# Optimization experiments

Measured on AMD Instinct MI355X. Metric: run time of the kernel, lower is better.

## Reference

```python
import jax, jax.numpy as jnp
import numpy as np

F_, H_, W_ = 6, 16, 28          # latent video grid (frames, height, width)
DIM, NH = 1536, 12
HD = DIM // NH                   # 128
L = F_ * H_ * W_                 # 2688 tokens
EPS = 1e-6
BLOCK = 3 * H_ * W_              # block_causal_size = 3*frame_height*frame_width


def setup_inputs() -> dict:
    key = jax.random.key(0)
    ks = jax.random.split(key, 8)
    def lin(k):
        return jax.random.normal(k, (DIM, DIM), jnp.float32) * 0.02
    x = jax.random.normal(ks[0], (1, L, DIM), jnp.float32)
    # RoPE freqs: unit-modulus complex numbers stored as [...,(re,im)]
    ang = jax.random.uniform(ks[1], (1024, HD // 2), jnp.float32, -np.pi, np.pi)
    freqs = jnp.stack([jnp.cos(ang), jnp.sin(ang)], axis=-1)  # [1024, 64, 2]
    return {
        'x': x,
        'seq_lens': jnp.array([L], jnp.int32),
        'grid_sizes': jnp.array([[F_, H_, W_]], jnp.int32),
        'freqs': freqs,
        'Wq': lin(ks[2]), 'bq': jnp.zeros((DIM,), jnp.float32),
        'Wk': lin(ks[3]), 'bk': jnp.zeros((DIM,), jnp.float32),
        'Wv': lin(ks[4]), 'bv': jnp.zeros((DIM,), jnp.float32),
        'Wo': lin(ks[5]), 'bo': jnp.zeros((DIM,), jnp.float32),
        'gq': jnp.ones((DIM,), jnp.float32),
        'gk': jnp.ones((DIM,), jnp.float32),
    }


def _rmsnorm(x, g):
    # WanRMSNorm: x * rsqrt(mean(x^2) + eps) * weight
    return x * jax.lax.rsqrt(jnp.mean(x * x, axis=-1, keepdims=True) + EPS) * g


def _rope_apply(x, F, H, W, freqs, start_frame=0):
    # x: [B, L, n, d]; freqs: [1024, d//2, 2] (re, im). Per-axis split [c0, c3, c3].
    B, Lx, n, d = x.shape
    c = d // 2
    c3 = c // 3
    c0 = c - 2 * c3
    f0 = freqs[start_frame:start_frame + F, :c0]      # [F, c0, 2]
    f1 = freqs[:H, c0:c0 + c3]                        # [H, c3, 2]
    f2 = freqs[:W, c0 + c3:]                          # [W, c3, 2]
    ff = jnp.concatenate([
        jnp.broadcast_to(f0[:, None, None], (F, H, W, c0, 2)),
        jnp.broadcast_to(f1[None, :, None], (F, H, W, c3, 2)),
        jnp.broadcast_to(f2[None, None, :], (F, H, W, c3, 2)),
    ], axis=3).reshape(Lx, 1, c, 2)                   # [L, 1, c, 2]
    xr = x.reshape(B, Lx, n, c, 2)
    xre, xim = xr[..., 0], xr[..., 1]
    fre, fim = ff[None, ..., 0], ff[None, ..., 1]     # broadcast over batch, heads
    ore = xre * fre - xim * fim
    oim = xre * fim + xim * fre
    return jnp.stack([ore, oim], axis=-1).reshape(B, Lx, n, d)


def reference(x, seq_lens, grid_sizes, freqs, Wq, bq, Wk, bk, Wv, bv, Wo, bo, gq, gk):
    b, s = x.shape[:2]
    F = int(grid_sizes[0, 0]); H = int(grid_sizes[0, 1]); W = int(grid_sizes[0, 2])
    q = _rmsnorm(x @ Wq + bq, gq).reshape(b, s, NH, HD)
    k = _rmsnorm(x @ Wk + bk, gk).reshape(b, s, NH, HD)
    v = (x @ Wv + bv).reshape(b, s, NH, HD)
    rq = _rope_apply(q, F, H, W, freqs)
    rk = _rope_apply(k, F, H, W, freqs)
    # block-causal attention: query attends to keys in same-or-earlier 3-frame block
    scores = jnp.einsum('bihd,bjhd->bhij', rq, rk) * (HD ** -0.5)
    blk = jnp.arange(s) // (3 * H * W)
    mask = blk[None, :] <= blk[:, None]               # [s, s]
    scores = jnp.where(mask[None, None], scores, -1e30)
    attn = jax.nn.softmax(scores, axis=-1)
    out = jnp.einsum('bhij,bjhd->bihd', attn, v).reshape(b, s, DIM)
    return out @ Wo + bo
```

## Files before the change

kernel.cpp:

```cpp
#include <hip/hip_runtime.h>

#define L_SEQ 2688
#define DIM   1536
#define NH    12
#define HD    128
#define BLK_TOK 1344
#define HW_   448
#define W_    28

typedef unsigned short u16;
typedef unsigned int   u32;
typedef __attribute__((ext_vector_type(4))) float f32x4;
typedef __attribute__((ext_vector_type(16))) float f32x16;
typedef __attribute__((ext_vector_type(8))) short s16x8;
typedef __attribute__((ext_vector_type(2))) int i32x2;
typedef __attribute__((ext_vector_type(4))) u32 u32x4;

__device__ __forceinline__ u16 f2b(float f) {
    u32 u = __builtin_bit_cast(u32, f);
    return (u16)((u + 0x7FFFu + ((u >> 16) & 1u)) >> 16);
}
__device__ __forceinline__ float b2f(u16 b) {
    return __builtin_bit_cast(float, (u32)b << 16);
}
__device__ __forceinline__ u32 cvt_pk_bf16(float lo, float hi) {
    u32 r;
    asm("v_cvt_pk_bf16_f32 %0, %1, %2" : "=v"(r) : "v"(lo), "v"(hi));
    return r;
}

__global__ __launch_bounds__(256) void k_cvt_x(const float* __restrict__ x,
                                               u16* __restrict__ xb, int n4) {
    int i = blockIdx.x * 256 + threadIdx.x;
    int stride = gridDim.x * 256;
    for (; i < n4; i += stride) {
        float4 v = ((const float4*)x)[i];
        ushort4 o;
        o.x = f2b(v.x); o.y = f2b(v.y); o.z = f2b(v.z); o.w = f2b(v.w);
        ((ushort4*)xb)[i] = o;
    }
}

__global__ __launch_bounds__(256) void k_trans_w(const float* __restrict__ w0,
                                                 const float* __restrict__ w1,
                                                 const float* __restrict__ w2,
                                                 const float* __restrict__ w3,
                                                 u16* __restrict__ wt_all) {
    const float* w = blockIdx.z == 0 ? w0 : blockIdx.z == 1 ? w1 : blockIdx.z == 2 ? w2 : w3;
    u16* wt = wt_all + (size_t)blockIdx.z * DIM * DIM;
    __shared__ float t[64][65];
    const int k0 = blockIdx.y * 64, n0 = blockIdx.x * 64;
    const int c = threadIdx.x & 63, rg = threadIdx.x >> 6;
#pragma unroll
    for (int it = 0; it < 16; ++it) {
        int r = rg * 16 + it;
        t[r][c] = w[(size_t)(k0 + r) * DIM + n0 + c];
    }
    __syncthreads();
#pragma unroll
    for (int it = 0; it < 16; ++it) {
        int r = rg * 16 + it;
        wt[(size_t)(n0 + r) * DIM + k0 + c] = f2b(t[c][r]);
    }
}

template<int OUTF>
__global__ __launch_bounds__(256, 2) void k_gemm(const u16* __restrict__ A,
                                                 const u16* __restrict__ Bt_all,
                                                 const float* __restrict__ b0,
                                                 const float* __restrict__ b1,
                                                 const float* __restrict__ b2,
                                                 void* __restrict__ out_all) {
    const int z = blockIdx.z;
    const u16* Bt = Bt_all + (size_t)z * DIM * DIM;
    const float* bias = z == 0 ? b0 : z == 1 ? b1 : b2;

    __shared__ u16 lA[128 * 32];
    __shared__ u16 lB[128 * 32];
    const int tid = threadIdx.x, lane = tid & 63, wid = tid >> 6;
    const int wm = wid >> 1, wn = wid & 1;
    const int bm = blockIdx.y, bn = blockIdx.x;
    const int lr = lane & 15, lg = lane >> 4;

    f32x4 acc[4][4] = {};

    for (int kt = 0; kt < DIM / 32; ++kt) {
#pragma unroll
        for (int i = 0; i < 2; ++i) {
            int s = wid * 128 + i * 64 + lane;
            int row = s >> 2, c16 = s & 3;
            const u16* ga = A + (size_t)(bm * 128 + row) * DIM + kt * 32 + c16 * 8;
            __builtin_amdgcn_global_load_lds(
                (const __attribute__((address_space(1))) u32*)ga,
                (__attribute__((address_space(3))) u32*)&lA[(wid * 128 + i * 64) * 8],
                16, 0, 0);
            const u16* gb = Bt + (size_t)(bn * 128 + row) * DIM + kt * 32 + c16 * 8;
            __builtin_amdgcn_global_load_lds(
                (const __attribute__((address_space(1))) u32*)gb,
                (__attribute__((address_space(3))) u32*)&lB[(wid * 128 + i * 64) * 8],
                16, 0, 0);
        }
        __syncthreads();
        s16x8 af[4], bf[4];
#pragma unroll
        for (int m = 0; m < 4; ++m)
            af[m] = *(const s16x8*)&lA[(wm * 64 + m * 16 + lr) * 32 + lg * 8];
#pragma unroll
        for (int n = 0; n < 4; ++n)
            bf[n] = *(const s16x8*)&lB[(wn * 64 + n * 16 + lr) * 32 + lg * 8];
#pragma unroll
        for (int m = 0; m < 4; ++m)
#pragma unroll
            for (int n = 0; n < 4; ++n)
                acc[m][n] = __builtin_amdgcn_mfma_f32_16x16x32_bf16(af[m], bf[n], acc[m][n], 0, 0, 0);
        __syncthreads();
    }
#pragma unroll
    for (int n = 0; n < 4; ++n) {
        int col = bn * 128 + wn * 64 + n * 16 + lr;
        float bv = bias[col];
#pragma unroll
        for (int m = 0; m < 4; ++m) {
            int row0 = bm * 128 + wm * 64 + m * 16 + lg * 4;
#pragma unroll
            for (int r = 0; r < 4; ++r) {
                float v = acc[m][n][r] + bv;
                if (OUTF)
                    ((float*)out_all)[(size_t)(row0 + r) * DIM + col] = v;
                else
                    ((u16*)out_all)[(size_t)z * L_SEQ * DIM + (size_t)(row0 + r) * DIM + col] = f2b(v);
            }
        }
    }
}

__global__ __launch_bounds__(256) void k_norm_rope(const u16* __restrict__ pre_all,
                                                   const float* __restrict__ gq,
                                                   const float* __restrict__ gk,
                                                   const float* __restrict__ freqs,
                                                   u16* __restrict__ qh,
                                                   u16* __restrict__ kh) {
    const int which = blockIdx.y;
    const u16* pre = pre_all + (size_t)which * L_SEQ * DIM;
    const float* g = which ? gk : gq;
    u16* outh = which ? kh : qh;

    const int i = blockIdx.x;
    const int t = threadIdx.x;
    const u32* prow = (const u32*)(pre + (size_t)i * DIM);

    float re[3], im[3];
    float ss = 0.f;
#pragma unroll
    for (int a = 0; a < 3; ++a) {
        u32 p = prow[t + a * 256];
        float x = b2f((u16)(p & 0xFFFFu)), y = b2f((u16)(p >> 16));
        re[a] = x; im[a] = y;
        ss += x * x + y * y;
    }
#pragma unroll
    for (int o = 32; o > 0; o >>= 1) ss += __shfl_down(ss, o, 64);
    __shared__ float sred[4];
    if ((t & 63) == 0) sred[t >> 6] = ss;
    __syncthreads();
    float rms = rsqrtf((sred[0] + sred[1] + sred[2] + sred[3]) * (1.0f / DIM) + 1e-6f);

    const int f = i / HW_;
    const int rem = i - f * HW_;
    const int hp = rem / W_;
    const int wp = rem - hp * W_;
#pragma unroll
    for (int a = 0; a < 3; ++a) {
        int j = t + a * 256;
        int h = j >> 6, pj = j & 63;
        float2 gg = ((const float2*)g)[j];
        float x = re[a] * rms * gg.x;
        float y = im[a] * rms * gg.y;
        int ridx = pj < 22 ? f : (pj < 43 ? hp : wp);
        float2 cs = ((const float2*)freqs)[ridx * 64 + pj];
        float ore = x * cs.x - y * cs.y;
        float oim = x * cs.y + y * cs.x;
        u32 o = (u32)f2b(ore) | ((u32)f2b(oim) << 16);
        ((u32*)outh)[(size_t)h * (L_SEQ * 64) + (size_t)i * 64 + pj] = o;
    }
}

__global__ __launch_bounds__(256) void k_vtrans(const u16* __restrict__ vpre,
                                                u16* __restrict__ vt) {
    const int i0 = blockIdx.x * 64, d0 = blockIdx.y * 64, h = blockIdx.z;
    __shared__ u16 t[64][68];
    const int c = threadIdx.x & 63, rg = threadIdx.x >> 6;
#pragma unroll
    for (int it = 0; it < 16; ++it) {
        int r = rg * 16 + it;
        t[r][c] = vpre[(size_t)(i0 + r) * DIM + h * HD + d0 + c];
    }
    __syncthreads();
#pragma unroll
    for (int it = 0; it < 16; ++it) {
        int r = rg * 16 + it;
        vt[(size_t)h * (HD * L_SEQ) + (size_t)(d0 + r) * L_SEQ + i0 + c] = t[c][r];
    }
}

__global__ __launch_bounds__(256, 2) void k_attn(const u16* __restrict__ qh,
                                                 const u16* __restrict__ kh,
                                                 const u16* __restrict__ vt,
                                                 u16* __restrict__ ob,
                                                 float* __restrict__ Opart,
                                                 float* __restrict__ mlp) {
    __shared__ char lsm[2][32768];

    const int flat = blockIdx.x;
    const int xcd = flat & 7, idx = flat >> 3;
    const int work = (xcd < 4) ? (xcd * 95 + idx) : (380 + (xcd - 4) * 94 + idx);
    const int head = work / 63;
    const int bx = work - head * 63;
    int qt, kv0, mode;
    if (bx < 21)      { qt = bx;      kv0 = 0;  mode = 0; }
    else if (bx < 42) { qt = bx;      kv0 = 0;  mode = 1; }
    else              { qt = bx - 21; kv0 = 21; mode = 2; }

    const int tid = threadIdx.x, lane = tid & 63, w = tid >> 6;
    const int pairI = w >> 1;
    const int qhalf = w & 1;
    const int q31 = lane & 31, hi = lane >> 5;
    const size_t hOff = (size_t)head * ((size_t)L_SEQ * HD);
    const u16* Kh = kh + hOff;
    const u16* Vh = vt + hOff;
    const int qrow0 = qt * 64 + qhalf * 32;

    s16x8 aq[8];
#pragma unroll
    for (int kk = 0; kk < 8; ++kk)
        aq[kk] = *(const s16x8*)&qh[hOff + (size_t)(qrow0 + q31) * HD + kk * 16 + hi * 8];

    const int rh = tid >> 4, ck = tid & 15;
    const int rv = tid >> 3, cv = tid & 7;
    const int koff = 8 * (ck ^ rh);
    const int voff = 8 * (cv ^ (rv & 7));

#define STAGE_TILE(TG, BUF)                                                       \
    {                                                                             \
        char* dst = lsm[BUF];                                                     \
        _Pragma("unroll")                                                         \
        for (int i = 0; i < 4; ++i) {                                             \
            const u16* src = Kh + (size_t)((TG) * 64 + i * 16 + rh) * HD + koff;  \
            __builtin_amdgcn_global_load_lds(                                     \
                (const __attribute__((address_space(1))) u32*)src,                \
                (__attribute__((address_space(3))) u32*)(dst + i * 4096 + tid * 16), 16, 0, 0); \
        }                                                                         \
        _Pragma("unroll")                                                         \
        for (int i = 0; i < 4; ++i) {                                             \
            const u16* src = Vh + (size_t)(i * 32 + rv) * L_SEQ + (TG) * 64 + voff; \
            __builtin_amdgcn_global_load_lds(                                     \
                (const __attribute__((address_space(1))) u32*)src,                \
                (__attribute__((address_space(3))) u32*)(dst + 16384 + i * 4096 + tid * 16), 16, 0, 0); \
        }                                                                         \
    }

    f32x16 acc[4] = {};
    float mrun = -1e30f, lrun = 0.f;
    const float sc2 = 0.12751739646917983f;
    const int krow = pairI * 32 + q31;

    STAGE_TILE(kv0, 0);
    __syncthreads();
    for (int t = 0; t < 21; ++t) {
        if (t < 20) STAGE_TILE(kv0 + t + 1, (t + 1) & 1);
        const char* slot = lsm[t & 1];

        f32x16 sv = {};
        __builtin_amdgcn_s_setprio(1);
#pragma unroll
        for (int kk = 0; kk < 8; ++kk) {
            int off = krow * 256 + ((kk * 32 + hi * 16) ^ ((q31 & 15) << 4));
            s16x8 kf = *(const s16x8*)(slot + off);
            sv = __builtin_amdgcn_mfma_f32_32x32x16_bf16(kf, aq[kk], sv, 0, 0, 0);
        }
        __builtin_amdgcn_s_setprio(0);

        float mx = sv[0];
#pragma unroll
        for (int e = 1; e < 16; ++e) mx = fmaxf(mx, sv[e]);
        mx = fmaxf(mx, __shfl_xor(mx, 32, 64));
        mx *= sc2;
        const int resc = (mx - mrun) > 11.5f;
        const float mm = resc ? mx : mrun;
        const float fac = resc ? __builtin_amdgcn_exp2f(mrun - mm) : 1.0f;
        mrun = mm;
        float sum = 0.f;
#pragma unroll
        for (int e = 0; e < 16; ++e) {
            float pv = __builtin_amdgcn_exp2f(sv[e] * sc2 - mm);
            sv[e] = pv;
            sum += pv;
        }
        sum += __shfl_xor(sum, 32, 64);
        lrun = lrun * fac + sum;
        if (__any(resc)) {
#pragma unroll
            for (int ds = 0; ds < 4; ++ds)
#pragma unroll
                for (int e = 0; e < 16; ++e) acc[ds][e] *= fac;
        }

        s16x8 pa[2];
#pragma unroll
        for (int hf = 0; hf < 2; ++hf) {
            u32 a0 = cvt_pk_bf16(sv[hf * 8 + 0], sv[hf * 8 + 1]);
            u32 a1 = cvt_pk_bf16(sv[hf * 8 + 2], sv[hf * 8 + 3]);
            u32 b0 = cvt_pk_bf16(sv[hf * 8 + 4], sv[hf * 8 + 5]);
            u32 b1 = cvt_pk_bf16(sv[hf * 8 + 6], sv[hf * 8 + 7]);
            i32x2 r0 = __builtin_amdgcn_permlane32_swap((int)a0, (int)b0, false, false);
            i32x2 r1 = __builtin_amdgcn_permlane32_swap((int)a1, (int)b1, false, false);
            u32x4 fw;
            fw.x = (u32)r0.x; fw.y = (u32)r1.x; fw.z = (u32)r0.y; fw.w = (u32)r1.y;
            pa[hf] = __builtin_bit_cast(s16x8, fw);
        }

        __builtin_amdgcn_s_setprio(1);
#pragma unroll
        for (int jstep = 0; jstep < 2; ++jstep)
#pragma unroll
            for (int ds = 0; ds < 4; ++ds) {
                int off = 16384 + (ds * 32 + q31) * 128 +
                          ((pairI * 64 + jstep * 32 + hi * 16) ^ ((q31 & 7) << 4));
                s16x8 vf = *(const s16x8*)(slot + off);
                acc[ds] = __builtin_amdgcn_mfma_f32_32x32x16_bf16(vf, pa[jstep], acc[ds], 0, 0, 0);
            }
        __builtin_amdgcn_s_setprio(0);
        __syncthreads();
    }

    float2* mlb = (float2*)(lsm[1]);
    char* accb = lsm[0];
    if (w >= 2) {
        char* base = accb + qhalf * 16384 + lane * 256;
#pragma unroll
        for (int ds = 0; ds < 4; ++ds)
#pragma unroll
            for (int g = 0; g < 4; ++g) {
                f32x4 v4;
#pragma unroll
                for (int e = 0; e < 4; ++e) v4[e] = acc[ds][g * 4 + e];
                *(f32x4*)(base + (((ds * 4 + g) * 16) ^ ((lane & 15) << 4))) = v4;
            }
        if (hi == 0) {
            float2 t2; t2.x = mrun; t2.y = lrun;
            mlb[qhalf * 32 + q31] = t2;
        }
    }
    __syncthreads();
    if (w < 2) {
        float2 ml2 = mlb[qhalf * 32 + q31];
        float M = fmaxf(mrun, ml2.x);
        float wa = exp2f(mrun - M), wb = exp2f(ml2.x - M);
        lrun = lrun * wa + ml2.y * wb;
        mrun = M;
        const char* base = accb + qhalf * 16384 + lane * 256;
#pragma unroll
        for (int ds = 0; ds < 4; ++ds)
#pragma unroll
            for (int g = 0; g < 4; ++g) {
                f32x4 v4 = *(const f32x4*)(base + (((ds * 4 + g) * 16) ^ ((lane & 15) << 4)));
#pragma unroll
                for (int e = 0; e < 4; ++e) acc[ds][g * 4 + e] = acc[ds][g * 4 + e] * wa + v4[e] * wb;
            }
        if (mode == 0) {
            const float inv = 1.0f / lrun;
            u16* orow = ob + (size_t)(qrow0 + q31) * DIM + head * HD;
#pragma unroll
            for (int ds = 0; ds < 4; ++ds)
#pragma unroll
                for (int g = 0; g < 4; ++g) {
                    uint2 pk2;
                    pk2.x = cvt_pk_bf16(acc[ds][g * 4 + 0] * inv, acc[ds][g * 4 + 1] * inv);
                    pk2.y = cvt_pk_bf16(acc[ds][g * 4 + 2] * inv, acc[ds][g * 4 + 3] * inv);
                    *(uint2*)(orow + ds * 32 + g * 8 + hi * 4) = pk2;
                }
        } else {
            const int pairo = (head * 21 + (qt - 21)) * 2 + (mode - 1);
            float* Op = Opart + (size_t)pairo * (64 * 128);
            const int rowl = qhalf * 32 + q31;
#pragma unroll
            for (int ds = 0; ds < 4; ++ds)
#pragma unroll
                for (int g = 0; g < 4; ++g) {
                    float4 v4;
                    v4.x = acc[ds][g * 4 + 0]; v4.y = acc[ds][g * 4 + 1];
                    v4.z = acc[ds][g * 4 + 2]; v4.w = acc[ds][g * 4 + 3];
                    *(float4*)(&Op[rowl * 128 + ds * 32 + g * 8 + hi * 4]) = v4;
                }
            if (hi == 0) {
                float2 t2; t2.x = mrun; t2.y = lrun;
                ((float2*)mlp)[(size_t)pairo * 64 + rowl] = t2;
            }
        }
    }
#undef STAGE_TILE
}

__global__ __launch_bounds__(256) void k_merge(const float* __restrict__ Opart,
                                               const float* __restrict__ mlp,
                                               u16* __restrict__ ob) {
    const int b = blockIdx.x;
    const int qt2 = b % 21, head = b / 21;
    const int pair = head * 21 + qt2;
    const float* O0 = Opart + (size_t)pair * 2 * 8192;
    const float* O1 = O0 + 8192;
    const int tid = threadIdx.x;
    const int row = tid >> 2, cs = (tid & 3) * 32;
    float2 a = ((const float2*)mlp)[(size_t)pair * 2 * 64 + row];
    float2 c = ((const float2*)mlp)[(size_t)(pair * 2 + 1) * 64 + row];
    float M = fmaxf(a.x, c.x);
    float w0 = exp2f(a.x - M), w1 = exp2f(c.x - M);
    float inv = 1.0f / (w0 * a.y + w1 * c.y);
    w0 *= inv; w1 *= inv;
    const int rowg = BLK_TOK + qt2 * 64 + row;
    u32* orow = (u32*)(ob + (size_t)rowg * DIM + head * HD + cs);
    const float4* p0 = (const float4*)(O0 + row * 128 + cs);
    const float4* p1 = (const float4*)(O1 + row * 128 + cs);
#pragma unroll
    for (int u = 0; u < 8; ++u) {
        float4 x0 = p0[u], x1 = p1[u];
        float o0 = x0.x * w0 + x1.x * w1;
        float o1 = x0.y * w0 + x1.y * w1;
        float o2 = x0.z * w0 + x1.z * w1;
        float o3 = x0.w * w0 + x1.w * w1;
        orow[u * 2]     = (u32)f2b(o0) | ((u32)f2b(o1) << 16);
        orow[u * 2 + 1] = (u32)f2b(o2) | ((u32)f2b(o3) << 16);
    }
}

extern "C" void kernel_launch(void* const* d_in, const int* in_sizes, int n_in,
                              void* d_out, int out_size, void* d_ws, size_t ws_size,
                              hipStream_t stream) {
    const float* x     = (const float*)d_in[0];
    const float* freqs = (const float*)d_in[3];
    const float* Wq    = (const float*)d_in[4];
    const float* bq    = (const float*)d_in[5];
    const float* Wk    = (const float*)d_in[6];
    const float* bk    = (const float*)d_in[7];
    const float* Wv    = (const float*)d_in[8];
    const float* bv    = (const float*)d_in[9];
    const float* Wo    = (const float*)d_in[10];
    const float* bo    = (const float*)d_in[11];
    const float* gq    = (const float*)d_in[12];
    const float* gk    = (const float*)d_in[13];

    const size_t LD = (size_t)L_SEQ * DIM;
    u16* wt_all  = (u16*)d_ws;
    u16* xb      = wt_all + (size_t)4 * DIM * DIM;
    u16* pre_all = xb + LD;
    u16* qh      = pre_all + 3 * LD;
    u16* kh2     = qh + LD;
    u16* vt      = kh2 + LD;
    u16* ob      = vt + LD;
    float* Opart = (float*)pre_all;
    float* mlp   = Opart + (size_t)12 * 21 * 2 * 64 * 128;

    k_cvt_x<<<2016, 256, 0, stream>>>(x, xb, (int)(LD / 4));
    k_trans_w<<<dim3(24, 24, 4), 256, 0, stream>>>(Wq, Wk, Wv, Wo, wt_all);
    k_gemm<0><<<dim3(12, 21, 3), 256, 0, stream>>>(xb, wt_all, bq, bk, bv, pre_all);
    k_norm_rope<<<dim3(L_SEQ, 2), 256, 0, stream>>>(pre_all, gq, gk, freqs, qh, kh2);
    k_vtrans<<<dim3(42, 2, NH), 256, 0, stream>>>(pre_all + 2 * LD, vt);
    k_attn<<<dim3(756), 256, 0, stream>>>(qh, kh2, vt, ob, Opart, mlp);
    k_merge<<<dim3(252), 256, 0, stream>>>(Opart, mlp, ob);
    k_gemm<1><<<dim3(12, 21, 1), 256, 0, stream>>>(ob, wt_all + (size_t)3 * DIM * DIM, bo, bo, bo, d_out);
}
```

Before: 171.9 us.

## Double-buffer GEMM LDS tiles and switch to 32x32x16 MFMA

The projection GEMM now prefetches the next K tile into a second LDS buffer while computing on the current one, removing one barrier per iteration. It also moves to 32x32x16 bf16 MFMA with a k-major LDS layout, and raises wave priority around the MFMA block. The occupancy hint of 2 blocks per CU is dropped, and the doubled LDS footprint could reduce occupancy.

```diff
diff --git a/kernel.cpp b/kernel.cpp
--- a/kernel.cpp
+++ b/kernel.cpp
@@ -7,6 +7,7 @@
 #define BLK_TOK 1344
 #define HW_   448
 #define W_    28
+#define NKIT  48
 
 typedef unsigned short u16;
 typedef unsigned int   u32;
@@ -65,73 +66,88 @@
 }
 
 template<int OUTF>
-__global__ __launch_bounds__(256, 2) void k_gemm(const u16* __restrict__ A,
-                                                 const u16* __restrict__ Bt_all,
-                                                 const float* __restrict__ b0,
-                                                 const float* __restrict__ b1,
-                                                 const float* __restrict__ b2,
-                                                 void* __restrict__ out_all) {
+__global__ __launch_bounds__(256) void k_gemm(const u16* __restrict__ A,
+                                              const u16* __restrict__ Bt_all,
+                                              const float* __restrict__ b0,
+                                              const float* __restrict__ b1,
+                                              const float* __restrict__ b2,
+                                              void* __restrict__ out_all) {
     const int z = blockIdx.z;
     const u16* Bt = Bt_all + (size_t)z * DIM * DIM;
     const float* bias = z == 0 ? b0 : z == 1 ? b1 : b2;
 
-    __shared__ u16 lA[128 * 32];
-    __shared__ u16 lB[128 * 32];
+    __shared__ u16 lbuf[2][2][4096];
     const int tid = threadIdx.x, lane = tid & 63, wid = tid >> 6;
     const int wm = wid >> 1, wn = wid & 1;
     const int bm = blockIdx.y, bn = blockIdx.x;
-    const int lr = lane & 15, lg = lane >> 4;
-
-    f32x4 acc[4][4] = {};
-
-    for (int kt = 0; kt < DIM / 32; ++kt) {
-#pragma unroll
-        for (int i = 0; i < 2; ++i) {
-            int s = wid * 128 + i * 64 + lane;
-            int row = s >> 2, c16 = s & 3;
-            const u16* ga = A + (size_t)(bm * 128 + row) * DIM + kt * 32 + c16 * 8;
-            __builtin_amdgcn_global_load_lds(
-                (const __attribute__((address_space(1))) u32*)ga,
-                (__attribute__((address_space(3))) u32*)&lA[(wid * 128 + i * 64) * 8],
-                16, 0, 0);
-            const u16* gb = Bt + (size_t)(bn * 128 + row) * DIM + kt * 32 + c16 * 8;
-            __builtin_amdgcn_global_load_lds(
-                (const __attribute__((address_space(1))) u32*)gb,
-                (__attribute__((address_space(3))) u32*)&lB[(wid * 128 + i * 64) * 8],
-                16, 0, 0);
-        }
+    const int q31 = lane & 31, hi = lane >> 5;
+
+    const int srow = tid & 127;
+    const u16* aRow = A  + (size_t)(bm * 128 + srow) * DIM + (tid >> 7) * 8;
+    const u16* bRow = Bt + (size_t)(bn * 128 + srow) * DIM + (tid >> 7) * 8;
+
+#define GSTAGE(KT, BUF)                                                            \
+    {                                                                              \
+        _Pragma("unroll")                                                          \
+        for (int i = 0; i < 2; ++i)                                                \
+            __builtin_amdgcn_global_load_lds(                                      \
+                (const __attribute__((address_space(1))) u32*)(aRow + (KT) * 32 + i * 16), \
+                (__attribute__((address_space(3))) u32*)((char*)&lbuf[BUF][0][0] + i * 4096 + tid * 16), \
+                16, 0, 0);                                                         \
+        _Pragma("unroll")                                                          \
+        for (int i = 0; i < 2; ++i)                                                \
+            __builtin_amdgcn_global_load_lds(                                      \
+                (const __attribute__((address_space(1))) u32*)(bRow + (KT) * 32 + i * 16), \
+                (__attribute__((address_space(3))) u32*)((char*)&lbuf[BUF][1][0] + i * 4096 + tid * 16), \
+                16, 0, 0);                                                         \
+    }
+
+    f32x16 acc[2][2] = {};
+
+    GSTAGE(0, 0);
+    __syncthreads();
+    for (int kt = 0; kt < NKIT; ++kt) {
+        if (kt < NKIT - 1) GSTAGE(kt + 1, (kt + 1) & 1);
+        const char* bufA = (const char*)&lbuf[kt & 1][0][0];
+        const char* bufB = (const char*)&lbuf[kt & 1][1][0];
+        s16x8 af[2][2], bf[2][2];
+#pragma unroll
+        for (int f = 0; f < 2; ++f)
+#pragma unroll
+            for (int kk = 0; kk < 2; ++kk) {
+                af[f][kk] = *(const s16x8*)(bufA + (2 * kk + hi) * 2048 + (wm * 64 + f * 32 + q31) * 16);
+                bf[f][kk] = *(const s16x8*)(bufB + (2 * kk + hi) * 2048 + (wn * 64 + f * 32 + q31) * 16);
+            }
+        __builtin_amdgcn_s_setprio(1);
+#pragma unroll
+        for (int kk = 0; kk < 2; ++kk)
+#pragma unroll
+            for (int fm = 0; fm < 2; ++fm)
+#pragma unroll
+                for (int fn = 0; fn < 2; ++fn)
+                    acc[fm][fn] = __builtin_amdgcn_mfma_f32_32x32x16_bf16(af[fm][kk], bf[fn][kk], acc[fm][fn], 0, 0, 0);
+        __builtin_amdgcn_s_setprio(0);
         __syncthreads();
-        s16x8 af[4], bf[4];
-#pragma unroll
-        for (int m = 0; m < 4; ++m)
-            af[m] = *(const s16x8*)&lA[(wm * 64 + m * 16 + lr) * 32 + lg * 8];
-#pragma unroll
-        for (int n = 0; n < 4; ++n)
-            bf[n] = *(const s16x8*)&lB[(wn * 64 + n * 16 + lr) * 32 + lg * 8];
-#pragma unroll
-        for (int m = 0; m < 4; ++m)
-#pragma unroll
-            for (int n = 0; n < 4; ++n)
-                acc[m][n] = __builtin_amdgcn_mfma_f32_16x16x32_bf16(af[m], bf[n], acc[m][n], 0, 0, 0);
-        __syncthreads();
-    }
-#pragma unroll
-    for (int n = 0; n < 4; ++n) {
-        int col = bn * 128 + wn * 64 + n * 16 + lr;
-        float bv = bias[col];
-#pragma unroll
-        for (int m = 0; m < 4; ++m) {
-            int row0 = bm * 128 + wm * 64 + m * 16 + lg * 4;
-#pragma unroll
-            for (int r = 0; r < 4; ++r) {
-                float v = acc[m][n][r] + bv;
+    }
+
+#pragma unroll
+    for (int fn = 0; fn < 2; ++fn) {
+        const int col = bn * 128 + wn * 64 + fn * 32 + q31;
+        const float bv = bias[col];
+#pragma unroll
+        for (int fm = 0; fm < 2; ++fm) {
+#pragma unroll
+            for (int e = 0; e < 16; ++e) {
+                const int row = bm * 128 + wm * 64 + fm * 32 + (e & 3) + 8 * (e >> 2) + 4 * hi;
+                const float v = acc[fm][fn][e] + bv;
                 if (OUTF)
-                    ((float*)out_all)[(size_t)(row0 + r) * DIM + col] = v;
+                    ((float*)out_all)[(size_t)row * DIM + col] = v;
                 else
-                    ((u16*)out_all)[(size_t)z * L_SEQ * DIM + (size_t)(row0 + r) * DIM + col] = f2b(v);
-            }
-        }
-    }
+                    ((u16*)out_all)[(size_t)z * L_SEQ * DIM + (size_t)row * DIM + col] = f2b(v);
+            }
+        }
+    }
+#undef GSTAGE
 }
 
 __global__ __launch_bounds__(256) void k_norm_rope(const u16* __restrict__ pre_all,
```

Result: slower. 215.6 us (+25.4%).
